# Kernel optimization log

Measured on AMD Instinct MI355X. Metric: run time of the kernel, lower is better.

The kernel has to match this reference:

```python
import jax, jax.numpy as jnp
import numpy as np

B, S, DIM = 2, 2048, 2048
H, KVH = 16, 8
HD = DIM // H            # 128
WIN = 512                # sliding window size
GLOB = 64                # global tokens
NEG = -1000000000.0


def _alibi_slopes(n):
    cp2 = 2.0 ** jnp.floor(jnp.log2(jnp.float32(n)))
    base = 2.0 ** (-(2.0 ** (-(jnp.log2(cp2) - 3.0))))
    powers = jnp.arange(1, 1 + n, dtype=jnp.float32)
    return jnp.power(base, powers)  # [n]


def _rope_tables(head_dim, seq_len, dtype=jnp.float32, base=10000.0):
    half = head_dim // 2
    freqs = 1.0 / base ** (jnp.arange(0, half, dtype=dtype) / half)
    t = jnp.arange(seq_len, dtype=dtype)
    f = jnp.outer(t, freqs)                       # [S, half]
    return jnp.sin(f)[None, None], jnp.cos(f)[None, None]  # [1,1,S,half]


def _rotary(x, sin, cos):
    # x: [b,h,s,d]; nonstandard rotation per source module
    x1, x2 = jnp.split(x, 2, axis=-1)
    return jnp.concatenate([x1 * cos - x2 * sin, x1 * sin + x2 * cos], axis=-1)


def _window_mask(seq_len):
    # Faithful to create_sliding_window_mask: 0.0 inside window / global rows+cols, -1e9 elsewhere
    i = jnp.arange(seq_len)[:, None]
    j = jnp.arange(seq_len)[None, :]
    m = jnp.where(jnp.abs(i - j) <= WIN // 2, 0.0, NEG)
    m = jnp.where((i < GLOB) | (j < GLOB), 0.0, m)
    return m  # [S, S] float


def setup_inputs() -> dict:
    key = jax.random.key(0)
    k1, k2, k3, k4 = jax.random.split(key, 4)
    x = jax.random.normal(k1, (B, S, DIM), dtype=jnp.float32)
    Wq = jax.random.normal(k2, (DIM, DIM), dtype=jnp.float32) * 0.02
    Wkv = jax.random.normal(k3, (DIM, 2 * KVH * HD), dtype=jnp.float32) * 0.02
    Wo = jax.random.normal(k4, (DIM, DIM), dtype=jnp.float32) * 0.02
    bo = jnp.zeros((DIM,), dtype=jnp.float32)
    return {"x": x, "Wq": Wq, "Wkv": Wkv, "Wo": Wo, "bo": bo}


def reference(x, Wq, Wkv, Wo, bo):
    b, s, dim = x.shape
    # token-complexity gating on queries
    complexity = jax.nn.sigmoid(jnp.sum(jnp.abs(x), axis=-1, keepdims=True))  # [b,s,1]
    q = jnp.dot(x * complexity, Wq)       # [b,s,dim]
    kv = jnp.dot(x, Wkv)                  # [b,s,2*kv_dim]
    k, v = jnp.split(kv, 2, axis=-1)

    q = q.reshape(b, s, H, HD).transpose(0, 2, 1, 3)      # [b,H,s,d]
    k = k.reshape(b, s, KVH, HD).transpose(0, 2, 1, 3)    # [b,KVH,s,d]
    v = v.reshape(b, s, KVH, HD).transpose(0, 2, 1, 3)

    sin, cos = _rope_tables(HD, s, dtype=x.dtype)
    q = _rotary(q, sin, cos)
    k = _rotary(k, sin, cos)

    r = H // KVH
    k = jnp.repeat(k, r, axis=1)   # 'b h s d -> b (h r) s d'
    v = jnp.repeat(v, r, axis=1)

    scale = 1.0 / jnp.sqrt(jnp.float32(HD)).astype(x.dtype)
    qk = jnp.einsum('bhid,bhjd->bhij', q, k) * scale      # [b,H,s,s]

    # ALiBi bias
    slopes = _alibi_slopes(H)                             # [H]
    pos = jnp.arange(s)
    dist = -jnp.abs(pos[:, None] - pos[None, :]).astype(jnp.float32)  # [s,s]
    qk = qk + slopes[:, None, None] * dist                # broadcast over batch

    # Faithful to source: jnp.where(float_mask, qk, NEG) treats nonzero (-1e9,
    # i.e. OUTSIDE window) as True -> keeps qk; zero (inside window) -> NEG.
    m = _window_mask(s)
    qk = jnp.where(m != 0.0, qk, NEG)

    attn = jax.nn.softmax(qk, axis=-1)
    out = jnp.einsum('bhij,bhjd->bhid', attn, v)          # [b,H,s,d]
    out = out.transpose(0, 2, 1, 3).reshape(b, s, dim)
    out = jnp.dot(out, Wo) + bo
    return out
```

## Files before the change

kernel.cpp:

```cpp
#include <hip/hip_runtime.h>

#define DEVI static __device__ __forceinline__

typedef __attribute__((ext_vector_type(8))) short short8;
typedef __attribute__((ext_vector_type(4))) short short4v;
typedef __attribute__((ext_vector_type(4))) float f32x4;

DEVI float bf2f(short u) {
  union { unsigned u32; float f; } c;
  c.u32 = ((unsigned)(unsigned short)u) << 16;
  return c.f;
}
DEVI short f2bf(float f) {
  union { float f; unsigned u32; } c; c.f = f;
  unsigned x = c.u32;
  unsigned r = (x + 0x7FFFu + ((x >> 16) & 1u)) >> 16;
  return (short)(unsigned short)r;
}
DEVI float ex2(float x) {
  float r;
  asm("v_exp_f32 %0, %1" : "=v"(r) : "v"(x));
  return r;
}
DEVI unsigned cvtpk(float lo, float hi) {
  unsigned r;
  asm("v_cvt_pk_bf16_f32 %0, %1, %2" : "=v"(r) : "v"(lo), "v"(hi));
  return r;
}

DEVI void gload16(const void* g, void* l) {
  __builtin_amdgcn_global_load_lds(
      (__attribute__((address_space(1))) void*)(g),
      (__attribute__((address_space(3))) void*)(l), 16, 0, 0);
}

#define LOG2E 1.4426950408889634f
#define QSCALE 0.1275174470974102f

__global__ void prep_x_kernel(const float* __restrict__ x,
                              short* __restrict__ xq, short* __restrict__ xb) {
  int row = blockIdx.x, t = threadIdx.x;
  const float4* xr = (const float4*)(x + (size_t)row * 2048);
  float4 v0 = xr[t], v1 = xr[t + 256];
  float s = fabsf(v0.x) + fabsf(v0.y) + fabsf(v0.z) + fabsf(v0.w)
          + fabsf(v1.x) + fabsf(v1.y) + fabsf(v1.z) + fabsf(v1.w);
#pragma unroll
  for (int m = 1; m < 64; m <<= 1) s += __shfl_xor(s, m, 64);
  __shared__ float red[4];
  if ((t & 63) == 0) red[t >> 6] = s;
  __syncthreads();
  float tot = red[0] + red[1] + red[2] + red[3];
  float sc = 1.0f / (1.0f + expf(-tot));
  short4v q0, q1, b0, b1;
  q0[0] = f2bf(v0.x * sc); q0[1] = f2bf(v0.y * sc); q0[2] = f2bf(v0.z * sc); q0[3] = f2bf(v0.w * sc);
  q1[0] = f2bf(v1.x * sc); q1[1] = f2bf(v1.y * sc); q1[2] = f2bf(v1.z * sc); q1[3] = f2bf(v1.w * sc);
  b0[0] = f2bf(v0.x); b0[1] = f2bf(v0.y); b0[2] = f2bf(v0.z); b0[3] = f2bf(v0.w);
  b1[0] = f2bf(v1.x); b1[1] = f2bf(v1.y); b1[2] = f2bf(v1.z); b1[3] = f2bf(v1.w);
  size_t base = (size_t)row * 512;
  ((short4v*)xq)[base + t]       = q0;
  ((short4v*)xq)[base + t + 256] = q1;
  ((short4v*)xb)[base + t]       = b0;
  ((short4v*)xb)[base + t + 256] = b1;
}

__global__ void sincos_kernel(float* __restrict__ tsin, float* __restrict__ tcos) {
  int idx = blockIdx.x * 256 + threadIdx.x;
  int d = idx >> 11, s = idx & 2047;
  float freq = powf(10000.0f, -(float)d / 64.0f);
  float f = (float)s * freq;
  tsin[idx] = sinf(f);
  tcos[idx] = cosf(f);
}

__global__ void wtrans_kernel(const float* __restrict__ W0, const float* __restrict__ W1,
                              const float* __restrict__ W2,
                              short* __restrict__ T0, short* __restrict__ T1,
                              short* __restrict__ T2) {
  __shared__ __align__(16) short tile[64][68];
  const float* W = blockIdx.z == 0 ? W0 : (blockIdx.z == 1 ? W1 : W2);
  short* WT      = blockIdx.z == 0 ? T0 : (blockIdx.z == 1 ? T1 : T2);
  int n0 = blockIdx.x * 64, k0 = blockIdx.y * 64;
  int t = threadIdx.x;
  int tr = t >> 4, tc = t & 15;
#pragma unroll
  for (int p = 0; p < 4; ++p) {
    int r = p * 16 + tr;
    int c = tc * 4;
    float4 v = *(const float4*)&W[(size_t)(k0 + r) * 2048 + n0 + c];
    tile[c + 0][r] = f2bf(v.x);
    tile[c + 1][r] = f2bf(v.y);
    tile[c + 2][r] = f2bf(v.z);
    tile[c + 3][r] = f2bf(v.w);
  }
  __syncthreads();
#pragma unroll
  for (int p = 0; p < 4; ++p) {
    int n = p * 16 + tr;
    int c = tc * 4;
    *(short4v*)&WT[(size_t)(n0 + n) * 2048 + k0 + c] = *(const short4v*)&tile[n][c];
  }
}

template<int EPI>
__launch_bounds__(256, 2)
__global__ void gemm_kernel(const short* __restrict__ A, const short* __restrict__ BT,
                            void* __restrict__ Cout, short* __restrict__ aux,
                            const float* __restrict__ bias,
                            const float* __restrict__ tsin, const float* __restrict__ tcos,
                            int M, int N, int K) {
  __shared__ __align__(16) short As[2][128 * 64];
  __shared__ __align__(16) short Bs[2][128 * 64];
  const int tid = threadIdx.x;
  const int wid = tid >> 6, lane = tid & 63;
  const int nb = gridDim.x * gridDim.y;
  const int orig = blockIdx.y * gridDim.x + blockIdx.x;
  const int swz = (orig & 7) * (nb >> 3) + (orig >> 3);
  const int m0 = (swz / gridDim.x) * 128, n0 = (swz % gridDim.x) * 128;
  const int l15 = lane & 15, l4 = lane >> 4;
  const int sw7 = l15 & 7;
  const int T = K >> 6;

  auto STAGE = [&](int bi, int t) {
#pragma unroll
    for (int p = 0; p < 4; ++p) {
      int cid = p * 256 + tid;
      int row = cid >> 3, ch = cid & 7;
      int cole = (ch ^ (row & 7)) * 8;
      gload16(A + (size_t)(m0 + row) * K + t * 64 + cole, &As[bi][cid * 8]);
      gload16(BT + (size_t)(n0 + row) * K + t * 64 + cole, &Bs[bi][cid * 8]);
    }
  };

  f32x4 acc[2][8] = {};
  STAGE(0, 0);
  for (int t = 0; t < T; ++t) {
    const int cur = t & 1;
    if (t + 1 < T) {
      STAGE(cur ^ 1, t + 1);
      asm volatile("s_waitcnt vmcnt(8)" ::: "memory");
    } else {
      asm volatile("s_waitcnt vmcnt(0)" ::: "memory");
    }
    __builtin_amdgcn_s_barrier();
#pragma unroll
    for (int kk = 0; kk < 2; ++kk) {
      const int cc = ((kk * 4 + l4) ^ sw7) * 8;
      short8 af0 = *(const short8*)&As[cur][(wid * 32 + l15) * 64 + cc];
      short8 af1 = *(const short8*)&As[cur][(wid * 32 + 16 + l15) * 64 + cc];
      short8 bf0 = *(const short8*)&Bs[cur][(0 * 16 + l15) * 64 + cc];
      short8 bf1 = *(const short8*)&Bs[cur][(1 * 16 + l15) * 64 + cc];
      short8 bf2 = *(const short8*)&Bs[cur][(2 * 16 + l15) * 64 + cc];
      short8 bf3 = *(const short8*)&Bs[cur][(3 * 16 + l15) * 64 + cc];
      __builtin_amdgcn_s_setprio(1);
      acc[0][0] = __builtin_amdgcn_mfma_f32_16x16x32_bf16(af0, bf0, acc[0][0], 0, 0, 0);
      acc[1][0] = __builtin_amdgcn_mfma_f32_16x16x32_bf16(af1, bf0, acc[1][0], 0, 0, 0);
      acc[0][1] = __builtin_amdgcn_mfma_f32_16x16x32_bf16(af0, bf1, acc[0][1], 0, 0, 0);
      acc[1][1] = __builtin_amdgcn_mfma_f32_16x16x32_bf16(af1, bf1, acc[1][1], 0, 0, 0);
      acc[0][2] = __builtin_amdgcn_mfma_f32_16x16x32_bf16(af0, bf2, acc[0][2], 0, 0, 0);
      acc[1][2] = __builtin_amdgcn_mfma_f32_16x16x32_bf16(af1, bf2, acc[1][2], 0, 0, 0);
      acc[0][3] = __builtin_amdgcn_mfma_f32_16x16x32_bf16(af0, bf3, acc[0][3], 0, 0, 0);
      acc[1][3] = __builtin_amdgcn_mfma_f32_16x16x32_bf16(af1, bf3, acc[1][3], 0, 0, 0);
      __builtin_amdgcn_s_setprio(0);
      bf0 = *(const short8*)&Bs[cur][(4 * 16 + l15) * 64 + cc];
      bf1 = *(const short8*)&Bs[cur][(5 * 16 + l15) * 64 + cc];
      bf2 = *(const short8*)&Bs[cur][(6 * 16 + l15) * 64 + cc];
      bf3 = *(const short8*)&Bs[cur][(7 * 16 + l15) * 64 + cc];
      __builtin_amdgcn_s_setprio(1);
      acc[0][4] = __builtin_amdgcn_mfma_f32_16x16x32_bf16(af0, bf0, acc[0][4], 0, 0, 0);
      acc[1][4] = __builtin_amdgcn_mfma_f32_16x16x32_bf16(af1, bf0, acc[1][4], 0, 0, 0);
      acc[0][5] = __builtin_amdgcn_mfma_f32_16x16x32_bf16(af0, bf1, acc[0][5], 0, 0, 0);
      acc[1][5] = __builtin_amdgcn_mfma_f32_16x16x32_bf16(af1, bf1, acc[1][5], 0, 0, 0);
      acc[0][6] = __builtin_amdgcn_mfma_f32_16x16x32_bf16(af0, bf2, acc[0][6], 0, 0, 0);
      acc[1][6] = __builtin_amdgcn_mfma_f32_16x16x32_bf16(af1, bf2, acc[1][6], 0, 0, 0);
      acc[0][7] = __builtin_amdgcn_mfma_f32_16x16x32_bf16(af0, bf3, acc[0][7], 0, 0, 0);
      acc[1][7] = __builtin_amdgcn_mfma_f32_16x16x32_bf16(af1, bf3, acc[1][7], 0, 0, 0);
      __builtin_amdgcn_s_setprio(0);
    }
    __builtin_amdgcn_s_barrier();
  }

  if (EPI == 0) {
#pragma unroll
    for (int mi = 0; mi < 2; ++mi) {
#pragma unroll
      for (int ni = 0; ni < 8; ++ni) {
        int col = n0 + ni * 16 + l15;
        float badd = bias[col];
#pragma unroll
        for (int r = 0; r < 4; ++r) {
          int row = m0 + wid * 32 + mi * 16 + l4 * 4 + r;
          ((float*)Cout)[(size_t)row * N + col] = acc[mi][ni][r] + badd;
        }
      }
    }
  } else if (EPI == 1) {
    const int h = n0 >> 7;
    const int b = m0 >> 11;
    const int sb = (m0 & 2047) + wid * 32;
    short* qr = (short*)Cout;
    const size_t obase = ((size_t)(b * 16 + h) * 2048 + sb) * 128;
#pragma unroll
    for (int mi = 0; mi < 2; ++mi) {
      int srel = sb + mi * 16 + l4 * 4;
#pragma unroll
      for (int ni = 0; ni < 4; ++ni) {
        int d = ni * 16 + l15;
        float4 sn = *(const float4*)&tsin[d * 2048 + srel];
        float4 cs = *(const float4*)&tcos[d * 2048 + srel];
#pragma unroll
        for (int r = 0; r < 4; ++r) {
          float x1 = acc[mi][ni][r], x2 = acc[mi][ni + 4][r];
          float snr = (&sn.x)[r], csr = (&cs.x)[r];
          size_t ro = obase + (size_t)(mi * 16 + l4 * 4 + r) * 128;
          qr[ro + d]      = f2bf((x1 * csr - x2 * snr) * QSCALE);
          qr[ro + d + 64] = f2bf((x1 * snr + x2 * csr) * QSCALE);
        }
      }
    }
  } else {
    const int b = m0 >> 11;
    const int sb = (m0 & 2047) + wid * 32;
    if (n0 < 1024) {
      const int kvh = n0 >> 7;
      short* kr = (short*)Cout;
      const size_t obase = ((size_t)(b * 8 + kvh) * 2048 + sb) * 128;
#pragma unroll
      for (int mi = 0; mi < 2; ++mi) {
        int srel = sb + mi * 16 + l4 * 4;
#pragma unroll
        for (int ni = 0; ni < 4; ++ni) {
          int d = ni * 16 + l15;
          float4 sn = *(const float4*)&tsin[d * 2048 + srel];
          float4 cs = *(const float4*)&tcos[d * 2048 + srel];
#pragma unroll
          for (int r = 0; r < 4; ++r) {
            float x1 = acc[mi][ni][r], x2 = acc[mi][ni + 4][r];
            float snr = (&sn.x)[r], csr = (&cs.x)[r];
            size_t ro = obase + (size_t)(mi * 16 + l4 * 4 + r) * 128;
            kr[ro + d]      = f2bf(x1 * csr - x2 * snr);
            kr[ro + d + 64] = f2bf(x1 * snr + x2 * csr);
          }
        }
      }
    } else {
      const int kvh = (n0 - 1024) >> 7;
      short* vt = aux;
      const size_t vb = (size_t)(b * 8 + kvh) * 128;
#pragma unroll
      for (int mi = 0; mi < 2; ++mi) {
        int srel = sb + mi * 16 + l4 * 4;
#pragma unroll
        for (int ni = 0; ni < 8; ++ni) {
          int d = ni * 16 + l15;
          uint2 w;
          w.x = cvtpk(acc[mi][ni][0], acc[mi][ni][1]);
          w.y = cvtpk(acc[mi][ni][2], acc[mi][ni][3]);
          *(uint2*)&vt[(vb + d) * 2048 + srel] = w;
        }
      }
    }
  }
}

__launch_bounds__(512, 4)
__global__ void attn_kernel(const short* __restrict__ qr, const short* __restrict__ kr,
                            const short* __restrict__ vt, short* __restrict__ ob) {
  __shared__ __align__(16) short Ks[2][64 * 128];
  __shared__ __align__(16) short Vs[2][128 * 64];
  __shared__ __align__(16) short PL[8][16 * 64];
  const int tid = threadIdx.x;
  const int wid = tid >> 6, lane = tid & 63;
  const int l15 = lane & 15, l4 = lane >> 4;
  const int sw7 = l15 & 7;
  const int l4h = l4 >> 1, l4l = l4 & 1;
  const int f = blockIdx.x + (blockIdx.y << 4) + (blockIdx.z << 8);
  const int swb = (f & 7) * 64 + (f >> 3);
  const int qt = swb & 15, h = (swb >> 4) & 15, b = swb >> 8;
  const int kh = h >> 1;
  const int qb = qt * 128;
  const int q0 = qb + wid * 16;
  const float slope2 = exp2f(-0.5f * (float)(h + 1)) * LOG2E;
  const size_t qbase = ((size_t)(b * 16 + h) * 2048 + q0) * 128;
  const size_t kbase = ((size_t)(b * 8 + kh) * 2048) * 128;
  const size_t vbase = ((size_t)(b * 8 + kh) * 128) * 2048;
  short* pl = PL[wid];

  short8 aq[4];
#pragma unroll
  for (int kk = 0; kk < 4; ++kk)
    aq[kk] = *(const short8*)&qr[qbase + (size_t)l15 * 128 + kk * 32 + l4 * 8];

  f32x4 o[8] = {};
  float m_run = -1e30f, l_run = 0.0f;
  const int iq = q0 + l15;

  int lo0, n0t, lo1, n1t;
  if (qt == 0)      { lo0 = 0;   n0t = 32;          lo1 = 0; n1t = 0; }
  else if (qt == 1) { lo0 = 384; n0t = 26;          lo1 = 0; n1t = 0; }
  else {
    lo0 = 64;        n0t = 2 * qt - 3;
    lo1 = qb + 256;  n1t = (28 - 2 * qt > 0) ? (28 - 2 * qt) : 0;
  }
  const int nt = n0t + n1t;
  auto KV0 = [&](int i) { return i < n0t ? lo0 + i * 64 : lo1 + (i - n0t) * 64; };

  auto STAGE = [&](int bi, int kv0) {
#pragma unroll
    for (int i2 = 0; i2 < 2; ++i2) {
      int cid = i2 * 512 + tid;
      int krow = cid >> 4, kch = cid & 15;
      gload16(kr + kbase + (size_t)(kv0 + krow) * 128 + ((kch ^ (krow & 7)) * 8),
              &Ks[bi][cid * 8]);
    }
#pragma unroll
    for (int i2 = 0; i2 < 2; ++i2) {
      int cid = i2 * 512 + tid;
      int vrow = cid >> 3, vch = cid & 7;
      gload16(vt + vbase + (size_t)vrow * 2048 + kv0 + ((vch ^ (vrow & 7)) * 8),
              &Vs[bi][cid * 8]);
    }
  };

  STAGE(0, KV0(0));
  __syncthreads();
  int cur = 0;

  for (int it = 0; it < nt; ++it) {
    const int kv0 = KV0(it);
    if (it + 1 < nt) STAGE(cur ^ 1, KV0(it + 1));

    int mode;
    if (q0 + 15 < 64 || kv0 == 0) mode = 3;
    else if (kv0 <= q0 - 320)     mode = 1;
    else if (kv0 >= q0 + 272)     mode = 2;
    else                          mode = 0;

    if (mode != 3) {
      f32x4 sc[4];
#pragma unroll
      for (int jj = 0; jj < 4; ++jj) sc[jj] = (f32x4){0.f, 0.f, 0.f, 0.f};
      __builtin_amdgcn_s_setprio(1);
#pragma unroll
      for (int kk = 0; kk < 4; ++kk) {
#pragma unroll
        for (int jj = 0; jj < 4; ++jj) {
          short8 bk = *(const short8*)&Ks[cur][(jj * 16 + l15) * 128 + (((kk * 4 + l4) ^ sw7) * 8)];
          sc[jj] = __builtin_amdgcn_mfma_f32_16x16x32_bf16(bk, aq[kk], sc[jj], 0, 0, 0);
        }
      }
      __builtin_amdgcn_s_setprio(0);
      float pm = -1e30f;
      const float dbase = (float)(iq - kv0 - l4 * 4);
      if (mode == 0) {
#pragma unroll
        for (int jj = 0; jj < 4; ++jj) {
          float dj = dbase - 16.0f * jj;
#pragma unroll
          for (int r = 0; r < 4; ++r) {
            float d = dj - (float)r;
            float ad = fabsf(d);
            float v = fmaf(-slope2, ad, sc[jj][r]);
            v = (ad > 256.0f) ? v : -1e9f;
            sc[jj][r] = v;
            pm = fmaxf(pm, v);
          }
        }
      } else {
        const float sl = (mode == 1) ? -slope2 : slope2;
#pragma unroll
        for (int jj = 0; jj < 4; ++jj) {
          float dj = dbase - 16.0f * jj;
#pragma unroll
          for (int r = 0; r < 4; ++r) {
            float v = fmaf(sl, dj - (float)r, sc[jj][r]);
            sc[jj][r] = v;
            pm = fmaxf(pm, v);
          }
        }
      }
      pm = fmaxf(pm, __shfl_xor(pm, 16, 64));
      pm = fmaxf(pm, __shfl_xor(pm, 32, 64));
      if (!__all(pm <= m_run + 8.0f)) {
        float mn = fmaxf(m_run, pm);
        float corr = ex2(m_run - mn);
        l_run *= corr;
#pragma unroll
        for (int dn = 0; dn < 8; ++dn)
#pragma unroll
          for (int r = 0; r < 4; ++r) o[dn][r] *= corr;
        m_run = mn;
      }
      float psum = 0.0f;
#pragma unroll
      for (int jj = 0; jj < 4; ++jj) {
        float p0 = ex2(sc[jj][0] - m_run);
        float p1 = ex2(sc[jj][1] - m_run);
        float p2 = ex2(sc[jj][2] - m_run);
        float p3 = ex2(sc[jj][3] - m_run);
        psum += (p0 + p1) + (p2 + p3);
        uint2 w; w.x = cvtpk(p0, p1); w.y = cvtpk(p2, p3);
        int ad = l15 * 64 + (((jj * 2 + l4h) ^ sw7) * 8) + l4l * 4;
        *(uint2*)&pl[ad] = w;
      }
      psum += __shfl_xor(psum, 16, 64);
      psum += __shfl_xor(psum, 32, 64);
      l_run += psum;
      asm volatile("s_waitcnt lgkmcnt(0)" ::: "memory");
      __builtin_amdgcn_sched_barrier(0);
      __builtin_amdgcn_s_setprio(1);
#pragma unroll
      for (int c = 0; c < 2; ++c) {
        short8 pa = *(const short8*)&pl[l15 * 64 + (((c * 4 + l4) ^ sw7) * 8)];
#pragma unroll
        for (int dn = 0; dn < 8; ++dn) {
          short8 bv = *(const short8*)&Vs[cur][(dn * 16 + l15) * 64 + (((c * 4 + l4) ^ sw7) * 8)];
          o[dn] = __builtin_amdgcn_mfma_f32_16x16x32_bf16(bv, pa, o[dn], 0, 0, 0);
        }
      }
      __builtin_amdgcn_s_setprio(0);
    } else {
      float pm = -1e9f;
      if (!__all(pm <= m_run + 8.0f)) {
        float mn = fmaxf(m_run, pm);
        float corr = ex2(m_run - mn);
        l_run *= corr;
#pragma unroll
        for (int dn = 0; dn < 8; ++dn)
#pragma unroll
          for (int r = 0; r < 4; ++r) o[dn][r] *= corr;
        m_run = mn;
      }
      float pu = ex2(-1e9f - m_run);
      l_run += 64.0f * pu;
      unsigned uu = cvtpk(pu, pu);
      short8 pa;
      ((unsigned*)&pa)[0] = uu; ((unsigned*)&pa)[1] = uu;
      ((unsigned*)&pa)[2] = uu; ((unsigned*)&pa)[3] = uu;
      __builtin_amdgcn_s_setprio(1);
#pragma unroll
      for (int c = 0; c < 2; ++c) {
#pragma unroll
        for (int dn = 0; dn < 8; ++dn) {
          short8 bv = *(const short8*)&Vs[cur][(dn * 16 + l15) * 64 + (((c * 4 + l4) ^ sw7) * 8)];
          o[dn] = __builtin_amdgcn_mfma_f32_16x16x32_bf16(bv, pa, o[dn], 0, 0, 0);
        }
      }
      __builtin_amdgcn_s_setprio(0);
    }
    __syncthreads();
    cur ^= 1;
  }

  float inv = 1.0f / l_run;
  size_t rbase = ((size_t)(b * 2048 + iq) * 16 + h) * 128;
#pragma unroll
  for (int dn = 0; dn < 8; ++dn) {
    uint2 w;
    w.x = cvtpk(o[dn][0] * inv, o[dn][1] * inv);
    w.y = cvtpk(o[dn][2] * inv, o[dn][3] * inv);
    *(uint2*)&ob[rbase + dn * 16 + l4 * 4] = w;
  }
}

extern "C" void kernel_launch(void* const* d_in, const int* in_sizes, int n_in,
                              void* d_out, int out_size, void* d_ws, size_t ws_size,
                              hipStream_t stream) {
  const float* x   = (const float*)d_in[0];
  const float* Wq  = (const float*)d_in[1];
  const float* Wkv = (const float*)d_in[2];
  const float* Wo  = (const float*)d_in[3];
  const float* bo  = (const float*)d_in[4];
  float* out = (float*)d_out;

  char* ws = (char*)d_ws;
  size_t off = 0;
  auto alloc = [&](size_t bytes) -> void* {
    void* p = ws + off;
    off += (bytes + 255) & ~(size_t)255;
    return p;
  };
  float* tsin  = (float*)alloc(64 * 2048 * 4);
  float* tcos  = (float*)alloc(64 * 2048 * 4);
  short* WqT   = (short*)alloc((size_t)2048 * 2048 * 2);
  short* WkvT  = (short*)alloc((size_t)2048 * 2048 * 2);
  short* WoT   = (short*)alloc((size_t)2048 * 2048 * 2);
  short* xq    = (short*)alloc((size_t)4096 * 2048 * 2);
  short* xb    = (short*)alloc((size_t)4096 * 2048 * 2);
  short* qr    = (short*)alloc((size_t)2 * 16 * 2048 * 128 * 2);
  short* kr    = (short*)alloc((size_t)2 * 8 * 2048 * 128 * 2);
  short* vt    = (short*)alloc((size_t)2 * 8 * 2048 * 128 * 2);
  short* ob    = xq;

  prep_x_kernel<<<4096, 256, 0, stream>>>(x, xq, xb);
  sincos_kernel<<<512, 256, 0, stream>>>(tsin, tcos);
  wtrans_kernel<<<dim3(32, 32, 3), 256, 0, stream>>>(Wq, Wkv, Wo, WqT, WkvT, WoT);
  gemm_kernel<1><<<dim3(16, 32), 256, 0, stream>>>(xq, WqT, qr, nullptr, nullptr, tsin, tcos, 4096, 2048, 2048);
  gemm_kernel<2><<<dim3(16, 32), 256, 0, stream>>>(xb, WkvT, kr, vt, nullptr, tsin, tcos, 4096, 2048, 2048);
  attn_kernel<<<dim3(16, 16, 2), 512, 0, stream>>>(qr, kr, vt, ob);
  gemm_kernel<0><<<dim3(16, 32), 256, 0, stream>>>(ob, WoT, (void*)out, nullptr, bo, nullptr, nullptr, 4096, 2048, 2048);
  (void)in_sizes; (void)n_in; (void)out_size; (void)ws_size;
}
```

Before: 226.8 us.

## Merge prep kernels, fuse Q and KV GEMMs, pipeline PV MFMA with softmax

```diff
diff --git a/kernel.cpp b/kernel.cpp
--- a/kernel.cpp
+++ b/kernel.cpp
@@ -37,106 +37,94 @@
 #define LOG2E 1.4426950408889634f
 #define QSCALE 0.1275174470974102f
 
-__global__ void prep_x_kernel(const float* __restrict__ x,
-                              short* __restrict__ xq, short* __restrict__ xb) {
-  int row = blockIdx.x, t = threadIdx.x;
-  const float4* xr = (const float4*)(x + (size_t)row * 2048);
-  float4 v0 = xr[t], v1 = xr[t + 256];
-  float s = fabsf(v0.x) + fabsf(v0.y) + fabsf(v0.z) + fabsf(v0.w)
-          + fabsf(v1.x) + fabsf(v1.y) + fabsf(v1.z) + fabsf(v1.w);
-#pragma unroll
-  for (int m = 1; m < 64; m <<= 1) s += __shfl_xor(s, m, 64);
+__global__ void prep_kernel(const float* __restrict__ x, short* __restrict__ xq,
+                            short* __restrict__ xb, float* __restrict__ tsin,
+                            float* __restrict__ tcos,
+                            const float* __restrict__ Wq, const float* __restrict__ Wkv,
+                            const float* __restrict__ Wo, short* __restrict__ T0,
+                            short* __restrict__ T1, short* __restrict__ T2) {
   __shared__ float red[4];
-  if ((t & 63) == 0) red[t >> 6] = s;
-  __syncthreads();
-  float tot = red[0] + red[1] + red[2] + red[3];
-  float sc = 1.0f / (1.0f + expf(-tot));
-  short4v q0, q1, b0, b1;
-  q0[0] = f2bf(v0.x * sc); q0[1] = f2bf(v0.y * sc); q0[2] = f2bf(v0.z * sc); q0[3] = f2bf(v0.w * sc);
-  q1[0] = f2bf(v1.x * sc); q1[1] = f2bf(v1.y * sc); q1[2] = f2bf(v1.z * sc); q1[3] = f2bf(v1.w * sc);
-  b0[0] = f2bf(v0.x); b0[1] = f2bf(v0.y); b0[2] = f2bf(v0.z); b0[3] = f2bf(v0.w);
-  b1[0] = f2bf(v1.x); b1[1] = f2bf(v1.y); b1[2] = f2bf(v1.z); b1[3] = f2bf(v1.w);
-  size_t base = (size_t)row * 512;
-  ((short4v*)xq)[base + t]       = q0;
-  ((short4v*)xq)[base + t + 256] = q1;
-  ((short4v*)xb)[base + t]       = b0;
-  ((short4v*)xb)[base + t + 256] = b1;
-}
-
-__global__ void sincos_kernel(float* __restrict__ tsin, float* __restrict__ tcos) {
-  int idx = blockIdx.x * 256 + threadIdx.x;
-  int d = idx >> 11, s = idx & 2047;
-  float freq = powf(10000.0f, -(float)d / 64.0f);
-  float f = (float)s * freq;
-  tsin[idx] = sinf(f);
-  tcos[idx] = cosf(f);
-}
-
-__global__ void wtrans_kernel(const float* __restrict__ W0, const float* __restrict__ W1,
-                              const float* __restrict__ W2,
-                              short* __restrict__ T0, short* __restrict__ T1,
-                              short* __restrict__ T2) {
   __shared__ __align__(16) short tile[64][68];
-  const float* W = blockIdx.z == 0 ? W0 : (blockIdx.z == 1 ? W1 : W2);
-  short* WT      = blockIdx.z == 0 ? T0 : (blockIdx.z == 1 ? T1 : T2);
-  int n0 = blockIdx.x * 64, k0 = blockIdx.y * 64;
-  int t = threadIdx.x;
-  int tr = t >> 4, tc = t & 15;
-#pragma unroll
-  for (int p = 0; p < 4; ++p) {
-    int r = p * 16 + tr;
-    int c = tc * 4;
-    float4 v = *(const float4*)&W[(size_t)(k0 + r) * 2048 + n0 + c];
-    tile[c + 0][r] = f2bf(v.x);
-    tile[c + 1][r] = f2bf(v.y);
-    tile[c + 2][r] = f2bf(v.z);
-    tile[c + 3][r] = f2bf(v.w);
-  }
-  __syncthreads();
-#pragma unroll
-  for (int p = 0; p < 4; ++p) {
-    int n = p * 16 + tr;
-    int c = tc * 4;
-    *(short4v*)&WT[(size_t)(n0 + n) * 2048 + k0 + c] = *(const short4v*)&tile[n][c];
-  }
-}
-
-template<int EPI>
-__launch_bounds__(256, 2)
-__global__ void gemm_kernel(const short* __restrict__ A, const short* __restrict__ BT,
-                            void* __restrict__ Cout, short* __restrict__ aux,
-                            const float* __restrict__ bias,
-                            const float* __restrict__ tsin, const float* __restrict__ tcos,
-                            int M, int N, int K) {
-  __shared__ __align__(16) short As[2][128 * 64];
-  __shared__ __align__(16) short Bs[2][128 * 64];
-  const int tid = threadIdx.x;
+  const int bid = blockIdx.x, t = threadIdx.x;
+  if (bid < 4096) {
+    int row = bid;
+    const float4* xr = (const float4*)(x + (size_t)row * 2048);
+    float4 v0 = xr[t], v1 = xr[t + 256];
+    float s = fabsf(v0.x) + fabsf(v0.y) + fabsf(v0.z) + fabsf(v0.w)
+            + fabsf(v1.x) + fabsf(v1.y) + fabsf(v1.z) + fabsf(v1.w);
+#pragma unroll
+    for (int m = 1; m < 64; m <<= 1) s += __shfl_xor(s, m, 64);
+    if ((t & 63) == 0) red[t >> 6] = s;
+    __syncthreads();
+    float tot = red[0] + red[1] + red[2] + red[3];
+    float sc = 1.0f / (1.0f + expf(-tot));
+    short4v q0, q1, b0, b1;
+    q0[0] = f2bf(v0.x * sc); q0[1] = f2bf(v0.y * sc); q0[2] = f2bf(v0.z * sc); q0[3] = f2bf(v0.w * sc);
+    q1[0] = f2bf(v1.x * sc); q1[1] = f2bf(v1.y * sc); q1[2] = f2bf(v1.z * sc); q1[3] = f2bf(v1.w * sc);
+    b0[0] = f2bf(v0.x); b0[1] = f2bf(v0.y); b0[2] = f2bf(v0.z); b0[3] = f2bf(v0.w);
+    b1[0] = f2bf(v1.x); b1[1] = f2bf(v1.y); b1[2] = f2bf(v1.z); b1[3] = f2bf(v1.w);
+    size_t base = (size_t)row * 512;
+    ((short4v*)xq)[base + t]       = q0;
+    ((short4v*)xq)[base + t + 256] = q1;
+    ((short4v*)xb)[base + t]       = b0;
+    ((short4v*)xb)[base + t + 256] = b1;
+  } else if (bid < 4608) {
+    int idx = (bid - 4096) * 256 + t;
+    int d = idx >> 11, s2 = idx & 2047;
+    float freq = powf(10000.0f, -(float)d / 64.0f);
+    float f = (float)s2 * freq;
+    tsin[idx] = sinf(f);
+    tcos[idx] = cosf(f);
+  } else {
+    int wt = bid - 4608;
+    const float* W = (wt < 1024) ? Wq : (wt < 2048 ? Wkv : Wo);
+    short* WT      = (wt < 1024) ? T0 : (wt < 2048 ? T1 : T2);
+    int n0 = (wt & 31) * 64, k0 = ((wt >> 5) & 31) * 64;
+    int tr = t >> 4, tc = t & 15;
+#pragma unroll
+    for (int p = 0; p < 4; ++p) {
+      int r = p * 16 + tr;
+      int c = tc * 4;
+      float4 v = *(const float4*)&W[(size_t)(k0 + r) * 2048 + n0 + c];
+      tile[c + 0][r] = f2bf(v.x);
+      tile[c + 1][r] = f2bf(v.y);
+      tile[c + 2][r] = f2bf(v.z);
+      tile[c + 3][r] = f2bf(v.w);
+    }
+    __syncthreads();
+#pragma unroll
+    for (int p = 0; p < 4; ++p) {
+      int n = p * 16 + tr;
+      int c = tc * 4;
+      *(short4v*)&WT[(size_t)(n0 + n) * 2048 + k0 + c] = *(const short4v*)&tile[n][c];
+    }
+  }
+}
+
+DEVI void gemm_core(const short* __restrict__ A, const short* __restrict__ BT,
+                    int K, int m0, int n0, int tid,
+                    short* As0, short* As1, short* Bs0, short* Bs1,
+                    f32x4 (&acc)[2][8]) {
   const int wid = tid >> 6, lane = tid & 63;
-  const int nb = gridDim.x * gridDim.y;
-  const int orig = blockIdx.y * gridDim.x + blockIdx.x;
-  const int swz = (orig & 7) * (nb >> 3) + (orig >> 3);
-  const int m0 = (swz / gridDim.x) * 128, n0 = (swz % gridDim.x) * 128;
   const int l15 = lane & 15, l4 = lane >> 4;
   const int sw7 = l15 & 7;
   const int T = K >> 6;
-
-  auto STAGE = [&](int bi, int t) {
+  auto STAGE = [&](short* Asb, short* Bsb, int t) {
 #pragma unroll
     for (int p = 0; p < 4; ++p) {
       int cid = p * 256 + tid;
       int row = cid >> 3, ch = cid & 7;
       int cole = (ch ^ (row & 7)) * 8;
-      gload16(A + (size_t)(m0 + row) * K + t * 64 + cole, &As[bi][cid * 8]);
-      gload16(BT + (size_t)(n0 + row) * K + t * 64 + cole, &Bs[bi][cid * 8]);
+      gload16(A + (size_t)(m0 + row) * K + t * 64 + cole, Asb + cid * 8);
+      gload16(BT + (size_t)(n0 + row) * K + t * 64 + cole, Bsb + cid * 8);
     }
   };
-
-  f32x4 acc[2][8] = {};
-  STAGE(0, 0);
+  STAGE(As0, Bs0, 0);
   for (int t = 0; t < T; ++t) {
-    const int cur = t & 1;
+    short* Asc = (t & 1) ? As1 : As0;
+    short* Bsc = (t & 1) ? Bs1 : Bs0;
     if (t + 1 < T) {
-      STAGE(cur ^ 1, t + 1);
+      STAGE((t & 1) ? As0 : As1, (t & 1) ? Bs0 : Bs1, t + 1);
       asm volatile("s_waitcnt vmcnt(8)" ::: "memory");
     } else {
       asm volatile("s_waitcnt vmcnt(0)" ::: "memory");
@@ -145,12 +133,12 @@
 #pragma unroll
     for (int kk = 0; kk < 2; ++kk) {
       const int cc = ((kk * 4 + l4) ^ sw7) * 8;
-      short8 af0 = *(const short8*)&As[cur][(wid * 32 + l15) * 64 + cc];
-      short8 af1 = *(const short8*)&As[cur][(wid * 32 + 16 + l15) * 64 + cc];
-      short8 bf0 = *(const short8*)&Bs[cur][(0 * 16 + l15) * 64 + cc];
-      short8 bf1 = *(const short8*)&Bs[cur][(1 * 16 + l15) * 64 + cc];
-      short8 bf2 = *(const short8*)&Bs[cur][(2 * 16 + l15) * 64 + cc];
-      short8 bf3 = *(const short8*)&Bs[cur][(3 * 16 + l15) * 64 + cc];
+      short8 af0 = *(const short8*)&Asc[(wid * 32 + l15) * 64 + cc];
+      short8 af1 = *(const short8*)&Asc[(wid * 32 + 16 + l15) * 64 + cc];
+      short8 bf0 = *(const short8*)&Bsc[(0 * 16 + l15) * 64 + cc];
+      short8 bf1 = *(const short8*)&Bsc[(1 * 16 + l15) * 64 + cc];
+      short8 bf2 = *(const short8*)&Bsc[(2 * 16 + l15) * 64 + cc];
+      short8 bf3 = *(const short8*)&Bsc[(3 * 16 + l15) * 64 + cc];
       __builtin_amdgcn_s_setprio(1);
       acc[0][0] = __builtin_amdgcn_mfma_f32_16x16x32_bf16(af0, bf0, acc[0][0], 0, 0, 0);
       acc[1][0] = __builtin_amdgcn_mfma_f32_16x16x32_bf16(af1, bf0, acc[1][0], 0, 0, 0);
@@ -161,10 +149,10 @@
       acc[0][3] = __builtin_amdgcn_mfma_f32_16x16x32_bf16(af0, bf3, acc[0][3], 0, 0, 0);
       acc[1][3] = __builtin_amdgcn_mfma_f32_16x16x32_bf16(af1, bf3, acc[1][3], 0, 0, 0);
       __builtin_amdgcn_s_setprio(0);
-      bf0 = *(const short8*)&Bs[cur][(4 * 16 + l15) * 64 + cc];
-      bf1 = *(const short8*)&Bs[cur][(5 * 16 + l15) * 64 + cc];
-      bf2 = *(const short8*)&Bs[cur][(6 * 16 + l15) * 64 + cc];
-      bf3 = *(const short8*)&Bs[cur][(7 * 16 + l15) * 64 + cc];
+      bf0 = *(const short8*)&Bsc[(4 * 16 + l15) * 64 + cc];
+      bf1 = *(const short8*)&Bsc[(5 * 16 + l15) * 64 + cc];
+      bf2 = *(const short8*)&Bsc[(6 * 16 + l15) * 64 + cc];
+      bf3 = *(const short8*)&Bsc[(7 * 16 + l15) * 64 + cc];
       __builtin_amdgcn_s_setprio(1);
       acc[0][4] = __builtin_amdgcn_mfma_f32_16x16x32_bf16(af0, bf0, acc[0][4], 0, 0, 0);
       acc[1][4] = __builtin_amdgcn_mfma_f32_16x16x32_bf16(af1, bf0, acc[1][4], 0, 0, 0);
@@ -178,26 +166,33 @@
     }
     __builtin_amdgcn_s_barrier();
   }
-
-  if (EPI == 0) {
-#pragma unroll
-    for (int mi = 0; mi < 2; ++mi) {
-#pragma unroll
-      for (int ni = 0; ni < 8; ++ni) {
-        int col = n0 + ni * 16 + l15;
-        float badd = bias[col];
-#pragma unroll
-        for (int r = 0; r < 4; ++r) {
-          int row = m0 + wid * 32 + mi * 16 + l4 * 4 + r;
-          ((float*)Cout)[(size_t)row * N + col] = acc[mi][ni][r] + badd;
-        }
-      }
-    }
-  } else if (EPI == 1) {
+}
+
+__launch_bounds__(256, 2)
+__global__ void gemm_qkv_kernel(const short* __restrict__ xq, const short* __restrict__ WqT,
+                                const short* __restrict__ xb, const short* __restrict__ WkvT,
+                                short* __restrict__ qr, short* __restrict__ kr,
+                                short* __restrict__ vt,
+                                const float* __restrict__ tsin, const float* __restrict__ tcos) {
+  __shared__ __align__(16) short As[2][128 * 64];
+  __shared__ __align__(16) short Bs[2][128 * 64];
+  const int which = blockIdx.z;
+  const int tid = threadIdx.x;
+  const int nb = gridDim.x * gridDim.y;
+  const int orig = blockIdx.y * gridDim.x + blockIdx.x;
+  const int swz = (orig & 7) * (nb >> 3) + (orig >> 3);
+  const int m0 = (swz / gridDim.x) * 128, n0 = (swz % gridDim.x) * 128;
+  const short* A  = which ? xb : xq;
+  const short* BT = which ? WkvT : WqT;
+  f32x4 acc[2][8] = {};
+  gemm_core(A, BT, 2048, m0, n0, tid, &As[0][0], &As[1][0], &Bs[0][0], &Bs[1][0], acc);
+
+  const int wid = tid >> 6, lane = tid & 63;
+  const int l15 = lane & 15, l4 = lane >> 4;
+  const int b = m0 >> 11;
+  const int sb = (m0 & 2047) + wid * 32;
+  if (which == 0) {
     const int h = n0 >> 7;
-    const int b = m0 >> 11;
-    const int sb = (m0 & 2047) + wid * 32;
-    short* qr = (short*)Cout;
     const size_t obase = ((size_t)(b * 16 + h) * 2048 + sb) * 128;
 #pragma unroll
     for (int mi = 0; mi < 2; ++mi) {
@@ -218,11 +213,8 @@
       }
     }
   } else {
-    const int b = m0 >> 11;
-    const int sb = (m0 & 2047) + wid * 32;
     if (n0 < 1024) {
       const int kvh = n0 >> 7;
-      short* kr = (short*)Cout;
       const size_t obase = ((size_t)(b * 8 + kvh) * 2048 + sb) * 128;
 #pragma unroll
       for (int mi = 0; mi < 2; ++mi) {
@@ -244,7 +236,6 @@
       }
     } else {
       const int kvh = (n0 - 1024) >> 7;
-      short* vt = aux;
       const size_t vb = (size_t)(b * 8 + kvh) * 128;
 #pragma unroll
       for (int mi = 0; mi < 2; ++mi) {
@@ -257,6 +248,35 @@
           w.y = cvtpk(acc[mi][ni][2], acc[mi][ni][3]);
           *(uint2*)&vt[(vb + d) * 2048 + srel] = w;
         }
+      }
+    }
+  }
+}
+
+__launch_bounds__(256, 2)
+__global__ void gemm_out_kernel(const short* __restrict__ A, const short* __restrict__ BT,
+                                float* __restrict__ Cout, const float* __restrict__ bias) {
+  __shared__ __align__(16) short As[2][128 * 64];
+  __shared__ __align__(16) short Bs[2][128 * 64];
+  const int tid = threadIdx.x;
+  const int nb = gridDim.x * gridDim.y;
+  const int orig = blockIdx.y * gridDim.x + blockIdx.x;
+  const int swz = (orig & 7) * (nb >> 3) + (orig >> 3);
+  const int m0 = (swz / gridDim.x) * 128, n0 = (swz % gridDim.x) * 128;
+  f32x4 acc[2][8] = {};
+  gemm_core(A, BT, 2048, m0, n0, tid, &As[0][0], &As[1][0], &Bs[0][0], &Bs[1][0], acc);
+  const int wid = tid >> 6, lane = tid & 63;
+  const int l15 = lane & 15, l4 = lane >> 4;
+#pragma unroll
+  for (int mi = 0; mi < 2; ++mi) {
+#pragma unroll
+    for (int ni = 0; ni < 8; ++ni) {
+      int col = n0 + ni * 16 + l15;
+      float badd = bias[col];
+#pragma unroll
+      for (int r = 0; r < 4; ++r) {
+        int row = m0 + wid * 32 + mi * 16 + l4 * 4 + r;
+        Cout[(size_t)row * 2048 + col] = acc[mi][ni][r] + badd;
       }
     }
   }
@@ -392,32 +412,49 @@
       }
       float psum = 0.0f;
 #pragma unroll
-      for (int jj = 0; jj < 4; ++jj) {
-        float p0 = ex2(sc[jj][0] - m_run);
-        float p1 = ex2(sc[jj][1] - m_run);
-        float p2 = ex2(sc[jj][2] - m_run);
-        float p3 = ex2(sc[jj][3] - m_run);
+      for (int jj = 0; jj < 2; ++jj) {
+        float p0 = ex2(sc[jj][0] - m_run), p1 = ex2(sc[jj][1] - m_run);
+        float p2 = ex2(sc[jj][2] - m_run), p3 = ex2(sc[jj][3] - m_run);
         psum += (p0 + p1) + (p2 + p3);
         uint2 w; w.x = cvtpk(p0, p1); w.y = cvtpk(p2, p3);
-        int ad = l15 * 64 + (((jj * 2 + l4h) ^ sw7) * 8) + l4l * 4;
-        *(uint2*)&pl[ad] = w;
-      }
+        *(uint2*)&pl[l15 * 64 + (((jj * 2 + l4h) ^ sw7) * 8) + l4l * 4] = w;
+      }
+      asm volatile("s_waitcnt lgkmcnt(0)" ::: "memory");
+      __builtin_amdgcn_sched_barrier(0);
+      short8 pa = *(const short8*)&pl[l15 * 64 + ((l4 ^ sw7) * 8)];
+      short8 bv0[8];
+#pragma unroll
+      for (int dn = 0; dn < 8; ++dn)
+        bv0[dn] = *(const short8*)&Vs[cur][(dn * 16 + l15) * 64 + ((l4 ^ sw7) * 8)];
+      uint2 w2[2];
+#pragma unroll
+      for (int jj = 2; jj < 4; ++jj) {
+        float p0 = ex2(sc[jj][0] - m_run), p1 = ex2(sc[jj][1] - m_run);
+        float p2 = ex2(sc[jj][2] - m_run), p3 = ex2(sc[jj][3] - m_run);
+        psum += (p0 + p1) + (p2 + p3);
+        w2[jj - 2].x = cvtpk(p0, p1); w2[jj - 2].y = cvtpk(p2, p3);
+      }
+      __builtin_amdgcn_s_setprio(1);
+#pragma unroll
+      for (int dn = 0; dn < 8; ++dn)
+        o[dn] = __builtin_amdgcn_mfma_f32_16x16x32_bf16(bv0[dn], pa, o[dn], 0, 0, 0);
+      __builtin_amdgcn_s_setprio(0);
+#pragma unroll
+      for (int jj = 2; jj < 4; ++jj)
+        *(uint2*)&pl[l15 * 64 + (((jj * 2 + l4h) ^ sw7) * 8) + l4l * 4] = w2[jj - 2];
+      asm volatile("s_waitcnt lgkmcnt(0)" ::: "memory");
+      __builtin_amdgcn_sched_barrier(0);
+      pa = *(const short8*)&pl[l15 * 64 + (((4 + l4) ^ sw7) * 8)];
+      __builtin_amdgcn_s_setprio(1);
+#pragma unroll
+      for (int dn = 0; dn < 8; ++dn) {
+        short8 bv = *(const short8*)&Vs[cur][(dn * 16 + l15) * 64 + (((4 + l4) ^ sw7) * 8)];
+        o[dn] = __builtin_amdgcn_mfma_f32_16x16x32_bf16(bv, pa, o[dn], 0, 0, 0);
+      }
+      __builtin_amdgcn_s_setprio(0);
       psum += __shfl_xor(psum, 16, 64);
       psum += __shfl_xor(psum, 32, 64);
       l_run += psum;
-      asm volatile("s_waitcnt lgkmcnt(0)" ::: "memory");
-      __builtin_amdgcn_sched_barrier(0);
-      __builtin_amdgcn_s_setprio(1);
-#pragma unroll
-      for (int c = 0; c < 2; ++c) {
-        short8 pa = *(const short8*)&pl[l15 * 64 + (((c * 4 + l4) ^ sw7) * 8)];
-#pragma unroll
-        for (int dn = 0; dn < 8; ++dn) {
-          short8 bv = *(const short8*)&Vs[cur][(dn * 16 + l15) * 64 + (((c * 4 + l4) ^ sw7) * 8)];
-          o[dn] = __builtin_amdgcn_mfma_f32_16x16x32_bf16(bv, pa, o[dn], 0, 0, 0);
-        }
-      }
-      __builtin_amdgcn_s_setprio(0);
     } else {
       float pm = -1e9f;
       if (!__all(pm <= m_run + 8.0f)) {
@@ -491,12 +528,9 @@
   short* vt    = (short*)alloc((size_t)2 * 8 * 2048 * 128 * 2);
   short* ob    = xq;
 
-  prep_x_kernel<<<4096, 256, 0, stream>>>(x, xq, xb);
-  sincos_kernel<<<512, 256, 0, stream>>>(tsin, tcos);
-  wtrans_kernel<<<dim3(32, 32, 3), 256, 0, stream>>>(Wq, Wkv, Wo, WqT, WkvT, WoT);
-  gemm_kernel<1><<<dim3(16, 32), 256, 0, stream>>>(xq, WqT, qr, nullptr, nullptr, tsin, tcos, 4096, 2048, 2048);
-  gemm_kernel<2><<<dim3(16, 32), 256, 0, stream>>>(xb, WkvT, kr, vt, nullptr, tsin, tcos, 4096, 2048, 2048);
+  prep_kernel<<<7680, 256, 0, stream>>>(x, xq, xb, tsin, tcos, Wq, Wkv, Wo, WqT, WkvT, WoT);
+  gemm_qkv_kernel<<<dim3(16, 32, 2), 256, 0, stream>>>(xq, WqT, xb, WkvT, qr, kr, vt, tsin, tcos);
   attn_kernel<<<dim3(16, 16, 2), 512, 0, stream>>>(qr, kr, vt, ob);
-  gemm_kernel<0><<<dim3(16, 32), 256, 0, stream>>>(ob, WoT, (void*)out, nullptr, bo, nullptr, nullptr, 4096, 2048, 2048);
+  gemm_out_kernel<<<dim3(16, 32), 256, 0, stream>>>(ob, WoT, out, bo);
   (void)in_sizes; (void)n_in; (void)out_size; (void)ws_size;
 }
```

After: 229.6 us. No clear change (+1.3%).
